# Optimization experiments

Measured on AMD Instinct MI355X. Metric: run time of the kernel, lower is better.

Reference implementation:

```python
import jax, jax.numpy as jnp
import numpy as np

B, N, DIM, HID, MAXN = 2048, 65536, 256, 512, 64
MID_KEY = (MAXN + HID) // 2   # 288
MID_VAL = (DIM + HID) // 2    # 384
MID_DEC = (HID + DIM) // 2    # 384
MID_SZ  = (HID + 1) // 2      # 256

def _ln(x, g, b):
    m = x.mean(-1, keepdims=True)
    v = ((x - m) ** 2).mean(-1, keepdims=True)
    return (x - m) * jax.lax.rsqrt(v + 1e-5) * g + b

def _mish(x):
    return x * jnp.tanh(jax.nn.softplus(x))

def _mlp_ln(x, W1, b1, g, be, W2, b2):
    return _mish(_ln(x @ W1 + b1, g, be)) @ W2 + b2

def _mlp(x, W1, b1, W2, b2):
    return _mish(x @ W1 + b1) @ W2 + b2

def setup_inputs():
    key = jax.random.key(0)
    ks = iter(jax.random.split(key, 40))
    def rn(shape, s=0.05):
        return jax.random.normal(next(ks), shape, jnp.float32) * s
    x = jax.random.normal(next(ks), (N, DIM), jnp.float32)
    batch = jnp.sort(jax.random.randint(next(ks), (N,), 0, B)).astype(jnp.int32)
    z32 = lambda *s: jnp.zeros(s, jnp.float32)
    o32 = lambda *s: jnp.ones(s, jnp.float32)
    return dict(
        x=x, batch=batch, n_batches=B,
        e_rank_W=rn((DIM, 1)), e_rank_b=z32(1),
        e_card_W=rn((1, HID)), e_card_b=z32(HID),
        e_key_W1=rn((MAXN, MID_KEY)), e_key_b1=z32(MID_KEY), e_key_g=o32(MID_KEY), e_key_be=z32(MID_KEY),
        e_key_W2=rn((MID_KEY, HID)), e_key_b2=z32(HID),
        e_val_W1=rn((DIM, MID_VAL)), e_val_b1=z32(MID_VAL), e_val_g=o32(MID_VAL), e_val_be=z32(MID_VAL),
        e_val_W2=rn((MID_VAL, HID)), e_val_b2=z32(HID),
        d_key_W1=rn((MAXN, MID_KEY)), d_key_b1=z32(MID_KEY), d_key_g=o32(MID_KEY), d_key_be=z32(MID_KEY),
        d_key_W2=rn((MID_KEY, HID)), d_key_b2=z32(HID),
        d_dec_W1=rn((HID, MID_DEC)), d_dec_b1=z32(MID_DEC),
        d_dec_W2=rn((MID_DEC, DIM)), d_dec_b2=z32(DIM),
        d_size_W1=rn((HID, MID_SZ)), d_size_b1=z32(MID_SZ), d_size_g=o32(MID_SZ), d_size_be=z32(MID_SZ),
        d_size_W2=rn((MID_SZ, 1)), d_size_b2=z32(1),
    )

def reference(x, batch, n_batches, e_rank_W, e_rank_b, e_card_W, e_card_b,
              e_key_W1, e_key_b1, e_key_g, e_key_be, e_key_W2, e_key_b2,
              e_val_W1, e_val_b1, e_val_g, e_val_be, e_val_W2, e_val_b2,
              d_key_W1, d_key_b1, d_key_g, d_key_be, d_key_W2, d_key_b2,
              d_dec_W1, d_dec_b1, d_dec_W2, d_dec_b2,
              d_size_W1, d_size_b1, d_size_g, d_size_be, d_size_W2, d_size_b2):
    max_n = e_key_W1.shape[0]
    n_pts = x.shape[0]
    # ---- Encoder ----
    n = jax.ops.segment_sum(jnp.ones(n_pts, jnp.float32), batch, num_segments=n_batches).astype(jnp.int32)
    mag = jnp.abs(x @ e_rank_W + e_rank_b)[:, 0]                 # [N]
    sort_key = batch.astype(jnp.float32) * jnp.max(mag) + mag    # sort within each set by |rank|
    idx = jnp.argsort(sort_key)
    xs = x[idx]
    starts = jnp.cumsum(n) - n                                   # per-set offsets (batch is sorted)
    pos_idx = jnp.arange(n_pts) - starts[batch]                  # rank within each set
    pos = jax.nn.one_hot(pos_idx, max_n, dtype=x.dtype)
    y = _mlp_ln(xs, e_val_W1, e_val_b1, e_val_g, e_val_be, e_val_W2, e_val_b2) \
      * _mlp_ln(pos, e_key_W1, e_key_b1, e_key_g, e_key_be, e_key_W2, e_key_b2)
    z = jax.ops.segment_sum(y, batch, num_segments=n_batches) \
      + n.astype(jnp.float32)[:, None] @ e_card_W + e_card_b     # [B, HID]
    # ---- Decoder ----
    n_logits = _mlp_ln(z, d_size_W1, d_size_b1, d_size_g, d_size_be, d_size_W2, d_size_b2)  # [B, 1]
    n_dec = jnp.clip(jnp.round(n_logits[:, 0]), 0, max_n).astype(jnp.int32)
    keys = _mlp_ln(jnp.eye(max_n, dtype=x.dtype),                # onehot positions 0..max_n-1
                   d_key_W1, d_key_b1, d_key_g, d_key_be, d_key_W2, d_key_b2)  # [max_n, HID]
    zp = z[:, None, :] * keys[None, :, :]                        # [B, max_n, HID] (repeat_interleave -> dense+mask)
    xf = _mlp(zp, d_dec_W1, d_dec_b1, d_dec_W2, d_dec_b2)        # [B, max_n, DIM]
    mask = jnp.arange(max_n)[None, :] < n_dec[:, None]           # valid rows per set
    x_out = (xf * mask[..., None].astype(xf.dtype)).reshape(-1, xf.shape[-1])
    batch_out = jnp.repeat(jnp.arange(n_batches, dtype=jnp.int32), max_n)
    return x_out, batch_out, mask.reshape(-1)
```

## Files before the change

### kernel.cpp

```cpp
#include <hip/hip_runtime.h>

#define NPTS   65536
#define NB     2048
#define DIMX   256
#define HIDN   512
#define MAXNN  64
#define MIDK   288
#define MIDV   384
#define MIDD   384
#define MIDS   256

typedef unsigned short ushort_t;
typedef __attribute__((ext_vector_type(8))) short short8;
typedef __attribute__((ext_vector_type(4))) float f32x4;

__device__ __forceinline__ float mishf(float x) {
    float e = __expf(fminf(x, 30.f));
    float n = e * (e + 2.f);
    return x * n * __builtin_amdgcn_rcpf(n + 2.f);
}
__device__ __forceinline__ ushort_t f2bf(float f) {
    unsigned u = __float_as_uint(f);
    u += 0x7fffu + ((u >> 16) & 1u);
    return (ushort_t)(u >> 16);
}
__device__ __forceinline__ float bf2f(ushort_t h) {
    return __uint_as_float(((unsigned)h) << 16);
}
__device__ __forceinline__ void dma16(const void* g, void* lds) {
    __builtin_amdgcn_global_load_lds(
        (const __attribute__((address_space(1))) unsigned int*)g,
        (__attribute__((address_space(3))) unsigned int*)lds, 16, 0, 0);
}

__global__ __launch_bounds__(256)
void k_starts(const int* __restrict__ batch, int* __restrict__ starts,
              unsigned int* __restrict__ maxmag)
{
    int b = blockIdx.x * blockDim.x + threadIdx.x;
    if (b == 0) *maxmag = 0u;
    if (b <= NB) {
        int lo = 0, hi = NPTS;
        while (lo < hi) { int mid = (lo + hi) >> 1; if (batch[mid] < b) lo = mid + 1; else hi = mid; }
        starts[b] = lo;
    }
}

__global__ __launch_bounds__(256)
void k_mag(const float* __restrict__ x, const float* __restrict__ rW,
           const float* __restrict__ rb, float* __restrict__ mag,
           unsigned int* __restrict__ maxmag, ushort_t* __restrict__ xb)
{
    const int lane = threadIdx.x & 63;
    const int wave = threadIdx.x >> 6;
    const int gw = blockIdx.x * 4 + wave;
    float4 wv = *(const float4*)(rW + lane * 4);
    float bias = rb[0];
    float lmax = 0.f;
    for (int pt = gw; pt < NPTS; pt += 16384) {
        float4 xv = *(const float4*)(x + (size_t)pt * DIMX + lane * 4);
        ushort4 u;
        u.x = f2bf(xv.x); u.y = f2bf(xv.y); u.z = f2bf(xv.z); u.w = f2bf(xv.w);
        *(ushort4*)(xb + (size_t)pt * DIMX + lane * 4) = u;
        double d = (double)xv.x * wv.x + (double)xv.y * wv.y
                 + (double)xv.z * wv.z + (double)xv.w * wv.w;
        #pragma unroll
        for (int o = 32; o > 0; o >>= 1) d += __shfl_xor(d, o);
        float s = fabsf((float)(d + (double)bias));
        if (lane == 0) mag[pt] = s;
        lmax = fmaxf(lmax, s);
    }
    __shared__ float wm[4];
    if (lane == 0) wm[wave] = lmax;
    __syncthreads();
    if (threadIdx.x == 0) {
        float m = fmaxf(fmaxf(wm[0], wm[1]), fmaxf(wm[2], wm[3]));
        atomicMax(maxmag, __float_as_uint(m));
    }
}

__global__ __launch_bounds__(256)
void k_rank(const int* __restrict__ batch, const int* __restrict__ starts,
            const float* __restrict__ mag, const unsigned int* __restrict__ maxmag,
            int* __restrict__ kidx)
{
    int i = blockIdx.x * 256 + threadIdx.x;
    if (i >= NPTS) return;
    int b = batch[i];
    int s = starts[b], e = starts[b + 1];
    float M = __uint_as_float(*maxmag);
    float kb = __fmul_rn((float)b, M);
    float ki = __fadd_rn(kb, mag[i]);
    int r = 0;
    for (int j = s; j < e; ++j) {
        float kj = __fadd_rn(kb, mag[j]);
        r += (kj < ki) || (kj == ki && j < i);
    }
    kidx[i] = (r < MAXNN) ? r : MAXNN;
}

__global__ __launch_bounds__(512)
void k_table2(const float* __restrict__ eW1, const float* __restrict__ eb1,
              const float* __restrict__ eg, const float* __restrict__ ebe,
              const float* __restrict__ eW2, const float* __restrict__ eb2,
              const float* __restrict__ dW1, const float* __restrict__ db1,
              const float* __restrict__ dg, const float* __restrict__ dbe,
              const float* __restrict__ dW2, const float* __restrict__ db2,
              float* __restrict__ enc_tbl, float* __restrict__ dec_tbl)
{
    const int row = blockIdx.x;
    const int t = threadIdx.x;
    const float *W1, *b1, *g, *be, *W2, *b2; float* out; int wrow;
    if (row < 65) {
        W1 = eW1; b1 = eb1; g = eg; be = ebe; W2 = eW2; b2 = eb2;
        out = enc_tbl + row * HIDN; wrow = (row < 64) ? row : -1;
    } else {
        int r = row - 65;
        W1 = dW1; b1 = db1; g = dg; be = dbe; W2 = dW2; b2 = db2;
        out = dec_tbl + r * HIDN; wrow = r;
    }
    __shared__ float h[MIDK];
    __shared__ float red[512];
    float v = 0.f;
    if (t < MIDK) v = b1[t] + (wrow >= 0 ? W1[wrow * MIDK + t] : 0.f);
    red[t] = (t < MIDK) ? v : 0.f;
    __syncthreads();
    for (int o = 256; o > 0; o >>= 1) { if (t < o) red[t] += red[t + o]; __syncthreads(); }
    float m = red[0] / (float)MIDK;
    __syncthreads();
    float d = v - m;
    red[t] = (t < MIDK) ? d * d : 0.f;
    __syncthreads();
    for (int o = 256; o > 0; o >>= 1) { if (t < o) red[t] += red[t + o]; __syncthreads(); }
    float rs = rsqrtf(red[0] / (float)MIDK + 1e-5f);
    __syncthreads();
    if (t < MIDK) h[t] = mishf(d * rs * g[t] + be[t]);
    __syncthreads();
    float acc = b2[t];
    #pragma unroll 8
    for (int k = 0; k < MIDK; ++k) acc = fmaf(h[k], W2[k * HIDN + t], acc);
    out[t] = acc;
}

__global__ __launch_bounds__(256)
void k_card(const int* __restrict__ starts, const float* __restrict__ cardW,
            const float* __restrict__ cardb, float* __restrict__ z)
{
    int idx = blockIdx.x * 256 + threadIdx.x;
    int b = idx >> 9, c = idx & 511;
    float n = (float)(starts[b + 1] - starts[b]);
    z[idx] = fmaf(n, cardW[c], cardb[c]);
}

__global__ __launch_bounds__(256)
void k_size(const float* __restrict__ z, const float* __restrict__ W1,
            const float* __restrict__ b1, const float* __restrict__ g,
            const float* __restrict__ be, const float* __restrict__ W2,
            const float* __restrict__ b2, int* __restrict__ ndec)
{
    const int b0 = blockIdx.x * 4, t = threadIdx.x;
    __shared__ float zr[4][HIDN];
    __shared__ float red[4][256];
    #pragma unroll
    for (int gI = 0; gI < 4; ++gI) {
        zr[gI][t] = z[(b0 + gI) * HIDN + t];
        zr[gI][t + 256] = z[(b0 + gI) * HIDN + 256 + t];
    }
    __syncthreads();
    float acc[4];
    float bb1 = b1[t];
    #pragma unroll
    for (int gI = 0; gI < 4; ++gI) acc[gI] = bb1;
    #pragma unroll 8
    for (int k = 0; k < HIDN; ++k) {
        float wv = W1[k * MIDS + t];
        #pragma unroll
        for (int gI = 0; gI < 4; ++gI) acc[gI] = fmaf(zr[gI][k], wv, acc[gI]);
    }
    #pragma unroll
    for (int gI = 0; gI < 4; ++gI) red[gI][t] = acc[gI];
    __syncthreads();
    for (int o = 128; o > 0; o >>= 1) {
        if (t < o) {
            #pragma unroll
            for (int gI = 0; gI < 4; ++gI) red[gI][t] += red[gI][t + o];
        }
        __syncthreads();
    }
    float mm[4];
    #pragma unroll
    for (int gI = 0; gI < 4; ++gI) mm[gI] = red[gI][0] * (1.f / 256.f);
    __syncthreads();
    #pragma unroll
    for (int gI = 0; gI < 4; ++gI) { float d = acc[gI] - mm[gI]; red[gI][t] = d * d; }
    __syncthreads();
    for (int o = 128; o > 0; o >>= 1) {
        if (t < o) {
            #pragma unroll
            for (int gI = 0; gI < 4; ++gI) red[gI][t] += red[gI][t + o];
        }
        __syncthreads();
    }
    float rs[4];
    #pragma unroll
    for (int gI = 0; gI < 4; ++gI) rs[gI] = rsqrtf(red[gI][0] * (1.f / 256.f) + 1e-5f);
    __syncthreads();
    float w2 = W2[t], gg = g[t], bbe = be[t];
    #pragma unroll
    for (int gI = 0; gI < 4; ++gI) {
        float h = mishf((acc[gI] - mm[gI]) * rs[gI] * gg + bbe);
        red[gI][t] = h * w2;
    }
    __syncthreads();
    for (int o = 128; o > 0; o >>= 1) {
        if (t < o) {
            #pragma unroll
            for (int gI = 0; gI < 4; ++gI) red[gI][t] += red[gI][t + o];
        }
        __syncthreads();
    }
    if (t < 4) {
        float logit = red[t][0] + b2[0];
        float n = rintf(logit);
        n = fminf(fmaxf(n, 0.f), 64.f);
        ndec[b0 + t] = (int)n;
    }
}

__global__ __launch_bounds__(256)
void k_compact_pad(const int* __restrict__ ndec, int* __restrict__ rowmap,
                   int* __restrict__ cntpad)
{
    __shared__ int lcnt;
    const int t = threadIdx.x;
    if (t == 0) lcnt = 0;
    __syncthreads();
    for (int b = t; b < NB; b += 256) {
        int n = ndec[b];
        if (n > 0) {
            int base = atomicAdd(&lcnt, n);
            for (int p = 0; p < n; ++p) rowmap[base + p] = b * 64 + p;
        }
    }
    __syncthreads();
    int c = lcnt;
    int pad = (c + 127) & ~127;
    for (int i = c + t; i < pad; i += 256) rowmap[i] = -1;
    if (t == 0) *cntpad = pad;
}

__global__ __launch_bounds__(256)
void k_tail(const int* __restrict__ ndec, float* __restrict__ outb,
            float* __restrict__ outm)
{
    int r = blockIdx.x * 256 + threadIdx.x;
    if (r < NB * MAXNN) {
        outb[r] = (float)(r >> 6);
        outm[r] = ((r & 63) < ndec[r >> 6]) ? 1.f : 0.f;
    }
}

__global__ __launch_bounds__(256)
void k_wt_all(const float* __restrict__ W0, ushort_t* __restrict__ T0,
              const float* __restrict__ W1s, ushort_t* __restrict__ T1,
              const float* __restrict__ W2s, ushort_t* __restrict__ T2,
              const float* __restrict__ W3s, ushort_t* __restrict__ T3)
{
    int idx = blockIdx.x * 256 + threadIdx.x;
    const float* W; ushort_t* T; int N, K, off;
    if (idx < 98304)       { W = W0;  T = T0; K = 256; N = 384; off = idx; }
    else if (idx < 294912) { W = W1s; T = T1; K = 384; N = 512; off = idx - 98304; }
    else if (idx < 491520) { W = W2s; T = T2; K = 512; N = 384; off = idx - 294912; }
    else                   { W = W3s; T = T3; K = 384; N = 256; off = idx - 491520; }
    int k = off / N, n = off - k * N;
    T[(size_t)n * K + k] = f2bf(W[off]);
}

__global__ __launch_bounds__(512, 2)
void k_enc(const ushort_t* __restrict__ A, const ushort_t* __restrict__ B1t,
           const float* __restrict__ b1, const float* __restrict__ g,
           const float* __restrict__ be, const ushort_t* __restrict__ B2t,
           const float* __restrict__ b2, const float* __restrict__ tbl,
           const int* __restrict__ kidx, const int* __restrict__ batch,
           float* __restrict__ zout)
{
    const int m0 = blockIdx.x * 128;
    __shared__ __align__(16) char SMEM[132096];
    ushort_t* slab = (ushort_t*)SMEM;
    ushort_t* As   = slab;
    ushort_t* Bs   = slab + 8192;
    ushort_t* Bs2  = (ushort_t*)(SMEM + 98304);
    float*    yred = (float*)(SMEM + 98304);
    float*    ssum = (float*)(SMEM + 98304);
    float*    ssq  = ssum + 512;
    int*      barr = (int*)(SMEM + 131072);
    int*      karr = barr + 128;

    const int t = threadIdx.x;
    const int l = t & 63;
    const int w = t >> 6;
    const int l4 = (l >> 4) << 2;
    const int drow = l >> 3;
    const int dblk = (l & 7) ^ drow;

    const int wmA = (w >> 2) * 64;
    const int wqA = (w & 3) * 96;
    f32x4 acc[4][6];
    #pragma unroll
    for (int a = 0; a < 4; ++a)
        #pragma unroll
        for (int b = 0; b < 6; ++b) acc[a][b] = (f32x4)0.f;

    for (int k0 = 0; k0 < DIMX; k0 += 64) {
        #pragma unroll
        for (int ii = 0; ii < 2; ++ii) {
            int i = w * 2 + ii;
            dma16(A + (size_t)(m0 + i * 8 + drow) * DIMX + k0 + dblk * 8, &As[i * 512]);
        }
        #pragma unroll
        for (int ii = 0; ii < 6; ++ii) {
            int i = w * 6 + ii;
            dma16(B1t + (size_t)(i * 8 + drow) * DIMX + k0 + dblk * 8, &Bs[i * 512]);
        }
        __syncthreads();
        #pragma unroll
        for (int ks = 0; ks < 2; ++ks) {
            int kq = ks * 4 + (l >> 4);
            short8 af[4], bfr[6];
            #pragma unroll
            for (int fm = 0; fm < 4; ++fm) {
                int row = wmA + fm * 16 + (l & 15);
                af[fm] = *(const short8*)&As[row * 64 + ((kq ^ (row & 7)) << 3)];
            }
            #pragma unroll
            for (int fn = 0; fn < 6; ++fn) {
                int row = wqA + fn * 16 + (l & 15);
                bfr[fn] = *(const short8*)&Bs[row * 64 + ((kq ^ (row & 7)) << 3)];
            }
            #pragma unroll
            for (int fm = 0; fm < 4; ++fm)
                #pragma unroll
                for (int fn = 0; fn < 6; ++fn)
                    acc[fm][fn] = __builtin_amdgcn_mfma_f32_16x16x32_bf16(
                        af[fm], bfr[fn], acc[fm][fn], 0, 0, 0);
        }
        __syncthreads();
    }

    float bb[6], gg[6], bee[6];
    #pragma unroll
    for (int fn = 0; fn < 6; ++fn) {
        int col = wqA + fn * 16 + (l & 15);
        bb[fn] = b1[col]; gg[fn] = g[col]; bee[fn] = be[col];
    }
    #pragma unroll
    for (int fm = 0; fm < 4; ++fm)
        #pragma unroll
        for (int fn = 0; fn < 6; ++fn)
            #pragma unroll
            for (int j = 0; j < 4; ++j) acc[fm][fn][j] += bb[fn];

    #pragma unroll
    for (int fm = 0; fm < 4; ++fm) {
        #pragma unroll
        for (int j = 0; j < 4; ++j) {
            float s = 0.f, q = 0.f;
            #pragma unroll
            for (int fn = 0; fn < 6; ++fn) {
                float v = acc[fm][fn][j];
                s += v; q += v * v;
            }
            #pragma unroll
            for (int o = 1; o < 16; o <<= 1) {
                s += __shfl_xor(s, o);
                q += __shfl_xor(q, o);
            }
            if ((l & 15) == 0) {
                int r = wmA + fm * 16 + l4 + j;
                ssum[r * 4 + (w & 3)] = s;
                ssq[r * 4 + (w & 3)] = q;
            }
        }
    }
    if (t < 128) { barr[t] = batch[m0 + t]; karr[t] = kidx[m0 + t]; }
    __syncthreads();

    #pragma unroll
    for (int fm = 0; fm < 4; ++fm) {
        #pragma unroll
        for (int j = 0; j < 4; ++j) {
            int r = wmA + fm * 16 + l4 + j;
            float s = ssum[r * 4 + 0] + ssum[r * 4 + 1] + ssum[r * 4 + 2] + ssum[r * 4 + 3];
            float q = ssq[r * 4 + 0] + ssq[r * 4 + 1] + ssq[r * 4 + 2] + ssq[r * 4 + 3];
            float m = s * (1.f / 384.f);
            float var = q * (1.f / 384.f) - m * m;
            float rs = rsqrtf(var + 1e-5f);
            #pragma unroll
            for (int fn = 0; fn < 6; ++fn) {
                float v = (acc[fm][fn][j] - m) * rs * gg[fn] + bee[fn];
                int c = wqA + fn * 16 + (l & 15);
                int panel = c >> 6, cc = c & 63;
                int kb = (cc >> 3) ^ (r & 7);
                slab[panel * 8192 + r * 64 + kb * 8 + (cc & 7)] = f2bf(mishf(v));
            }
        }
    }
    __syncthreads();

    const int wmB = (w >> 1) * 32;
    const int wnB = (w & 1) * 64;
    for (int nt = 0; nt < 4; ++nt) {
        const int n0t = nt * 128;
        f32x4 acc2[2][4];
        #pragma unroll
        for (int a = 0; a < 2; ++a)
            #pragma unroll
            for (int b = 0; b < 4; ++b) acc2[a][b] = (f32x4)0.f;

        for (int k0 = 0; k0 < MIDV; k0 += 64) {
            const int panel = k0 >> 6;
            #pragma unroll
            for (int ii = 0; ii < 2; ++ii) {
                int i = w * 2 + ii;
                dma16(B2t + (size_t)(n0t + i * 8 + drow) * MIDV + k0 + dblk * 8,
                      &Bs2[i * 512]);
            }
            __syncthreads();
            #pragma unroll
            for (int ks = 0; ks < 2; ++ks) {
                int kq = ks * 4 + (l >> 4);
                short8 af[2], bfr[4];
                #pragma unroll
                for (int fm = 0; fm < 2; ++fm) {
                    int row = wmB + fm * 16 + (l & 15);
                    af[fm] = *(const short8*)&slab[panel * 8192 + row * 64
                                                   + ((kq ^ (row & 7)) << 3)];
                }
                #pragma unroll
                for (int fn = 0; fn < 4; ++fn) {
                    int row = wnB + fn * 16 + (l & 15);
                    bfr[fn] = *(const short8*)&Bs2[row * 64 + ((kq ^ (row & 7)) << 3)];
                }
                #pragma unroll
                for (int fm = 0; fm < 2; ++fm)
                    #pragma unroll
                    for (int fn = 0; fn < 4; ++fn)
                        acc2[fm][fn] = __builtin_amdgcn_mfma_f32_16x16x32_bf16(
                            af[fm], bfr[fn], acc2[fm][fn], 0, 0, 0);
            }
            __syncthreads();
        }

        #pragma unroll
        for (int ph = 0; ph < 2; ++ph) {
            if ((w >> 2) == ph) {
                int rowbase = ((w >> 1) & 1) * 32;
                #pragma unroll
                for (int fn = 0; fn < 4; ++fn) {
                    int cl = wnB + fn * 16 + (l & 15);
                    float bbv = b2[n0t + cl];
                    #pragma unroll
                    for (int fm = 0; fm < 2; ++fm) {
                        #pragma unroll
                        for (int j = 0; j < 4; ++j) {
                            int rl = rowbase + fm * 16 + l4 + j;
                            int rg = ph * 64 + rl;
                            float v = (acc2[fm][fn][j] + bbv)
                                    * tbl[karr[rg] * HIDN + n0t + cl];
                            yred[cl * 64 + (rl ^ (cl & 31))] = v;
                        }
                    }
                }
            }
            __syncthreads();
            {
                int c = t & 127, q4 = t >> 7;
                int gc = n0t + c;
                float run = 0.f; int curb = -1;
                #pragma unroll 1
                for (int rr = 0; rr < 16; ++rr) {
                    int rl = q4 * 16 + rr;
                    int b = barr[ph * 64 + rl];
                    float v = yred[c * 64 + (rl ^ (c & 31))];
                    if (b != curb) {
                        if (curb >= 0) atomicAdd(&zout[curb * HIDN + gc], run);
                        curb = b; run = v;
                    } else run += v;
                }
                atomicAdd(&zout[curb * HIDN + gc], run);
            }
            __syncthreads();
        }
    }
}

template<int MODE>
__device__ __forceinline__
void mm_body(const ushort_t* __restrict__ A, const ushort_t* __restrict__ Bt,
             const float* __restrict__ bias, void* __restrict__ Cptr, int K,
             const float* __restrict__ tbl, const float* __restrict__ zin,
             const int* __restrict__ rowmap, const int* __restrict__ cntpad)
{
    const int flat = blockIdx.y * gridDim.x + blockIdx.x;
    const int nx = gridDim.x;
    const int xcd = flat & 7;
    const int lin = flat >> 3;
    const int n0 = (lin % nx) * 128;
    const int m0 = ((lin / nx) + ((gridDim.y >> 3) * xcd)) * 128;
    if (m0 >= *cntpad) return;
    __shared__ __align__(16) ushort_t sAB[2 * 128 * 64];
    ushort_t* As = sAB;
    ushort_t* Bs = sAB + 128 * 64;
    const int t = threadIdx.x;
    const int l = t & 63;
    const int w = t >> 6;
    const int wm = (w >> 1) * 64;
    const int wn = (w & 1) * 64;
    const int l4 = (l >> 4) << 2;
    const int drow = l >> 3;
    const int dblk = (l & 7) ^ drow;

    int g4[4], p4[4];
    if (MODE == 2) {
        #pragma unroll
        for (int ii = 0; ii < 4; ++ii) {
            int i = w * 4 + ii;
            int gr = rowmap[m0 + i * 8 + drow];
            if (gr < 0) gr = 0;
            g4[ii] = gr >> 6; p4[ii] = gr & 63;
        }
    }

    f32x4 acc[4][4];
    #pragma unroll
    for (int a = 0; a < 4; ++a)
        #pragma unroll
        for (int b = 0; b < 4; ++b) acc[a][b] = (f32x4)0.f;

    for (int k0 = 0; k0 < K; k0 += 64) {
        if (MODE == 2) {
            #pragma unroll
            for (int ii = 0; ii < 4; ++ii) {
                int i = w * 4 + ii;
                int row = i * 8 + drow;
                const float* zp = zin + g4[ii] * HIDN + k0 + dblk * 8;
                const float* kp = tbl + p4[ii] * HIDN + k0 + dblk * 8;
                float4 z0 = *(const float4*)zp;
                float4 z1 = *(const float4*)(zp + 4);
                float4 q0 = *(const float4*)kp;
                float4 q1 = *(const float4*)(kp + 4);
                ushort4 u0, u1;
                u0.x = f2bf(z0.x * q0.x); u0.y = f2bf(z0.y * q0.y);
                u0.z = f2bf(z0.z * q0.z); u0.w = f2bf(z0.w * q0.w);
                u1.x = f2bf(z1.x * q1.x); u1.y = f2bf(z1.y * q1.y);
                u1.z = f2bf(z1.z * q1.z); u1.w = f2bf(z1.w * q1.w);
                ushort_t* dst = &As[row * 64 + (l & 7) * 8];
                *(ushort4*)dst = u0;
                *(ushort4*)(dst + 4) = u1;
            }
        } else {
            #pragma unroll
            for (int ii = 0; ii < 4; ++ii) {
                int i = w * 4 + ii;
                const ushort_t* gp = A + (size_t)(m0 + i * 8 + drow) * K + k0 + dblk * 8;
                dma16(gp, &As[i * 512]);
            }
        }
        #pragma unroll
        for (int ii = 0; ii < 4; ++ii) {
            int i = w * 4 + ii;
            const ushort_t* gp = Bt + (size_t)(n0 + i * 8 + drow) * K + k0 + dblk * 8;
            dma16(gp, &Bs[i * 512]);
        }
        __syncthreads();
        #pragma unroll
        for (int ks = 0; ks < 2; ++ks) {
            short8 af[4], bfr[4];
            int kq = ks * 4 + (l >> 4);
            #pragma unroll
            for (int fm = 0; fm < 4; ++fm) {
                int row = wm + fm * 16 + (l & 15);
                af[fm] = *(const short8*)&As[row * 64 + ((kq ^ (row & 7)) << 3)];
            }
            #pragma unroll
            for (int fn = 0; fn < 4; ++fn) {
                int row = wn + fn * 16 + (l & 15);
                bfr[fn] = *(const short8*)&Bs[row * 64 + ((kq ^ (row & 7)) << 3)];
            }
            #pragma unroll
            for (int fm = 0; fm < 4; ++fm)
                #pragma unroll
                for (int fn = 0; fn < 4; ++fn)
                    acc[fm][fn] = __builtin_amdgcn_mfma_f32_16x16x32_bf16(
                        af[fm], bfr[fn], acc[fm][fn], 0, 0, 0);
        }
        __syncthreads();
    }

    if (MODE == 2) {
        ushort_t* C = (ushort_t*)Cptr;
        #pragma unroll
        for (int fm = 0; fm < 4; ++fm) {
            int gr0 = m0 + wm + fm * 16 + l4;
            #pragma unroll
            for (int fn = 0; fn < 4; ++fn) {
                int gc = n0 + wn + fn * 16 + (l & 15);
                float bbv = bias[gc];
                #pragma unroll
                for (int j = 0; j < 4; ++j)
                    C[(size_t)(gr0 + j) * MIDD + gc] = f2bf(mishf(acc[fm][fn][j] + bbv));
            }
        }
    } else {
        float* C = (float*)Cptr;
        #pragma unroll
        for (int fm = 0; fm < 4; ++fm) {
            int gr0 = m0 + wm + fm * 16 + l4;
            int om[4];
            #pragma unroll
            for (int j = 0; j < 4; ++j) om[j] = rowmap[gr0 + j];
            #pragma unroll
            for (int fn = 0; fn < 4; ++fn) {
                int gc = n0 + wn + fn * 16 + (l & 15);
                float bbv = bias[gc];
                #pragma unroll
                for (int j = 0; j < 4; ++j)
                    if (om[j] >= 0) C[(size_t)om[j] * DIMX + gc] = acc[fm][fn][j] + bbv;
            }
        }
    }
}

__global__ __launch_bounds__(256, 2)
void k_mm_d1(const ushort_t* Bt, const float* bias, void* C, int K,
             const float* tbl, const float* zin, const int* rowmap, const int* cntpad)
{ mm_body<2>(nullptr, Bt, bias, C, K, tbl, zin, rowmap, cntpad); }

__global__ __launch_bounds__(256, 2)
void k_mm_d2(const ushort_t* A, const ushort_t* Bt, const float* bias, void* C, int K,
             const int* rowmap, const int* cntpad)
{ mm_body<3>(A, Bt, bias, C, K, nullptr, nullptr, rowmap, cntpad); }

extern "C" void kernel_launch(void* const* d_in, const int* in_sizes, int n_in,
                              void* d_out, int out_size, void* d_ws, size_t ws_size,
                              hipStream_t stream)
{
    const float* x        = (const float*)d_in[0];
    const int*   batch    = (const int*)  d_in[1];
    const float* e_rank_W = (const float*)d_in[3];
    const float* e_rank_b = (const float*)d_in[4];
    const float* e_card_W = (const float*)d_in[5];
    const float* e_card_b = (const float*)d_in[6];
    const float* e_key_W1 = (const float*)d_in[7];
    const float* e_key_b1 = (const float*)d_in[8];
    const float* e_key_g  = (const float*)d_in[9];
    const float* e_key_be = (const float*)d_in[10];
    const float* e_key_W2 = (const float*)d_in[11];
    const float* e_key_b2 = (const float*)d_in[12];
    const float* e_val_W1 = (const float*)d_in[13];
    const float* e_val_b1 = (const float*)d_in[14];
    const float* e_val_g  = (const float*)d_in[15];
    const float* e_val_be = (const float*)d_in[16];
    const float* e_val_W2 = (const float*)d_in[17];
    const float* e_val_b2 = (const float*)d_in[18];
    const float* d_key_W1 = (const float*)d_in[19];
    const float* d_key_b1 = (const float*)d_in[20];
    const float* d_key_g  = (const float*)d_in[21];
    const float* d_key_be = (const float*)d_in[22];
    const float* d_key_W2 = (const float*)d_in[23];
    const float* d_key_b2 = (const float*)d_in[24];
    const float* d_dec_W1 = (const float*)d_in[25];
    const float* d_dec_b1 = (const float*)d_in[26];
    const float* d_dec_W2 = (const float*)d_in[27];
    const float* d_dec_b2 = (const float*)d_in[28];
    const float* d_size_W1= (const float*)d_in[29];
    const float* d_size_b1= (const float*)d_in[30];
    const float* d_size_g = (const float*)d_in[31];
    const float* d_size_be= (const float*)d_in[32];
    const float* d_size_W2= (const float*)d_in[33];
    const float* d_size_b2= (const float*)d_in[34];

    char* ws = (char*)d_ws;
    int*          starts  = (int*)         (ws + 0);
    unsigned int* maxmag  = (unsigned int*)(ws + 8448);
    int*          kidx    = (int*)         (ws + 8704);
    float*        mag     = (float*)       (ws + 270848);
    float*        enc_tbl = (float*)       (ws + 532992);
    float*        dec_tbl = (float*)       (ws + 666112);
    float*        z       = (float*)       (ws + 797184);
    int*          ndec    = (int*)         (ws + 4991488);
    int*          cntpad  = (int*)         (ws + 4999684);
    int*          rowmap  = (int*)         (ws + 5000192);
    ushort_t*     evW1t   = (ushort_t*)    (ws + 5524480);
    ushort_t*     evW2t   = (ushort_t*)    (ws + 5721088);
    ushort_t*     ddW1t   = (ushort_t*)    (ws + 6114304);
    ushort_t*     ddW2t   = (ushort_t*)    (ws + 6507520);
    ushort_t*     xb      = (ushort_t*)    (ws + 6704384);
    ushort_t*     Hd      = (ushort_t*)    (ws + 6704384 + 33554432);

    float* out_x = (float*)d_out;
    float* out_b = out_x + (size_t)NB * MAXNN * DIMX;
    float* out_m = out_b + NB * MAXNN;

    hipMemsetAsync(out_x, 0, (size_t)NB * MAXNN * DIMX * sizeof(float), stream);
    k_starts<<<dim3(9), dim3(256), 0, stream>>>(batch, starts, maxmag);
    k_mag<<<dim3(4096), dim3(256), 0, stream>>>(x, e_rank_W, e_rank_b, mag, maxmag, xb);
    k_rank<<<dim3(256), dim3(256), 0, stream>>>(batch, starts, mag, maxmag, kidx);
    k_table2<<<dim3(129), dim3(512), 0, stream>>>(
        e_key_W1, e_key_b1, e_key_g, e_key_be, e_key_W2, e_key_b2,
        d_key_W1, d_key_b1, d_key_g, d_key_be, d_key_W2, d_key_b2,
        enc_tbl, dec_tbl);
    k_card<<<dim3(4096), dim3(256), 0, stream>>>(starts, e_card_W, e_card_b, z);
    k_wt_all<<<dim3(2304), dim3(256), 0, stream>>>(e_val_W1, evW1t, e_val_W2, evW2t,
                                                   d_dec_W1, ddW1t, d_dec_W2, ddW2t);

    k_enc<<<dim3(512), dim3(512), 0, stream>>>(xb, evW1t, e_val_b1, e_val_g, e_val_be,
                                               evW2t, e_val_b2, enc_tbl, kidx, batch, z);

    k_size<<<dim3(NB / 4), dim3(256), 0, stream>>>(z, d_size_W1, d_size_b1, d_size_g,
                                                   d_size_be, d_size_W2, d_size_b2, ndec);
    k_compact_pad<<<dim3(1), dim3(256), 0, stream>>>(ndec, rowmap, cntpad);
    k_mm_d1<<<dim3(3, 1024), dim3(256), 0, stream>>>(ddW1t, d_dec_b1, Hd, HIDN,
                                                     dec_tbl, z, rowmap, cntpad);
    k_mm_d2<<<dim3(2, 1024), dim3(256), 0, stream>>>(Hd, ddW2t, d_dec_b2, out_x, MIDD,
                                                     rowmap, cntpad);
    k_tail<<<dim3(512), dim3(256), 0, stream>>>(ndec, out_b, out_m);
}
```

Measured before the change: 523.3 us.

## Merge setup kernels, inline segment bounds, widen encoder K step, batch segment-sum reads

```diff
diff --git a/kernel.cpp b/kernel.cpp
--- a/kernel.cpp
+++ b/kernel.cpp
@@ -32,18 +32,9 @@
         (const __attribute__((address_space(1))) unsigned int*)g,
         (__attribute__((address_space(3))) unsigned int*)lds, 16, 0, 0);
 }
-
-__global__ __launch_bounds__(256)
-void k_starts(const int* __restrict__ batch, int* __restrict__ starts,
-              unsigned int* __restrict__ maxmag)
-{
-    int b = blockIdx.x * blockDim.x + threadIdx.x;
-    if (b == 0) *maxmag = 0u;
-    if (b <= NB) {
-        int lo = 0, hi = NPTS;
-        while (lo < hi) { int mid = (lo + hi) >> 1; if (batch[mid] < b) lo = mid + 1; else hi = mid; }
-        starts[b] = lo;
-    }
+__device__ __forceinline__ int lbound(const int* __restrict__ a, int lo, int hi, int v) {
+    while (lo < hi) { int m = (lo + hi) >> 1; if (a[m] < v) lo = m + 1; else hi = m; }
+    return lo;
 }
 
 __global__ __launch_bounds__(256)
@@ -80,14 +71,14 @@
 }
 
 __global__ __launch_bounds__(256)
-void k_rank(const int* __restrict__ batch, const int* __restrict__ starts,
-            const float* __restrict__ mag, const unsigned int* __restrict__ maxmag,
-            int* __restrict__ kidx)
+void k_rank(const int* __restrict__ batch, const float* __restrict__ mag,
+            const unsigned int* __restrict__ maxmag, int* __restrict__ kidx)
 {
     int i = blockIdx.x * 256 + threadIdx.x;
     if (i >= NPTS) return;
     int b = batch[i];
-    int s = starts[b], e = starts[b + 1];
+    int s = lbound(batch, 0, NPTS, b);
+    int e = lbound(batch, s, NPTS, b + 1);
     float M = __uint_as_float(*maxmag);
     float kb = __fmul_rn((float)b, M);
     float ki = __fadd_rn(kb, mag[i]);
@@ -100,56 +91,69 @@
 }
 
 __global__ __launch_bounds__(512)
-void k_table2(const float* __restrict__ eW1, const float* __restrict__ eb1,
-              const float* __restrict__ eg, const float* __restrict__ ebe,
-              const float* __restrict__ eW2, const float* __restrict__ eb2,
-              const float* __restrict__ dW1, const float* __restrict__ db1,
-              const float* __restrict__ dg, const float* __restrict__ dbe,
-              const float* __restrict__ dW2, const float* __restrict__ db2,
-              float* __restrict__ enc_tbl, float* __restrict__ dec_tbl)
-{
-    const int row = blockIdx.x;
+void k_setup(const float* __restrict__ eW1, const float* __restrict__ eb1,
+             const float* __restrict__ eg, const float* __restrict__ ebe,
+             const float* __restrict__ eW2, const float* __restrict__ eb2,
+             const float* __restrict__ dW1, const float* __restrict__ db1,
+             const float* __restrict__ dg, const float* __restrict__ dbe,
+             const float* __restrict__ dW2, const float* __restrict__ db2,
+             float* __restrict__ enc_tbl, float* __restrict__ dec_tbl,
+             const int* __restrict__ batch, const float* __restrict__ cardW,
+             const float* __restrict__ cardb, float* __restrict__ z,
+             const float* __restrict__ V0, ushort_t* __restrict__ T0,
+             const float* __restrict__ V1, ushort_t* __restrict__ T1,
+             const float* __restrict__ V2, ushort_t* __restrict__ T2,
+             const float* __restrict__ V3, ushort_t* __restrict__ T3)
+{
+    const int blk = blockIdx.x;
     const int t = threadIdx.x;
-    const float *W1, *b1, *g, *be, *W2, *b2; float* out; int wrow;
-    if (row < 65) {
-        W1 = eW1; b1 = eb1; g = eg; be = ebe; W2 = eW2; b2 = eb2;
-        out = enc_tbl + row * HIDN; wrow = (row < 64) ? row : -1;
+    if (blk < 129) {
+        const float *W1, *b1, *g, *be, *W2, *b2; float* out; int wrow;
+        if (blk < 65) {
+            W1 = eW1; b1 = eb1; g = eg; be = ebe; W2 = eW2; b2 = eb2;
+            out = enc_tbl + blk * HIDN; wrow = (blk < 64) ? blk : -1;
+        } else {
+            int r = blk - 65;
+            W1 = dW1; b1 = db1; g = dg; be = dbe; W2 = dW2; b2 = db2;
+            out = dec_tbl + r * HIDN; wrow = r;
+        }
+        __shared__ float h[MIDK];
+        __shared__ float red[512];
+        float v = 0.f;
+        if (t < MIDK) v = b1[t] + (wrow >= 0 ? W1[wrow * MIDK + t] : 0.f);
+        red[t] = (t < MIDK) ? v : 0.f;
+        __syncthreads();
+        for (int o = 256; o > 0; o >>= 1) { if (t < o) red[t] += red[t + o]; __syncthreads(); }
+        float m = red[0] / (float)MIDK;
+        __syncthreads();
+        float d = v - m;
+        red[t] = (t < MIDK) ? d * d : 0.f;
+        __syncthreads();
+        for (int o = 256; o > 0; o >>= 1) { if (t < o) red[t] += red[t + o]; __syncthreads(); }
+        float rs = rsqrtf(red[0] / (float)MIDK + 1e-5f);
+        __syncthreads();
+        if (t < MIDK) h[t] = mishf(d * rs * g[t] + be[t]);
+        __syncthreads();
+        float acc = b2[t];
+        #pragma unroll 8
+        for (int k = 0; k < MIDK; ++k) acc = fmaf(h[k], W2[k * HIDN + t], acc);
+        out[t] = acc;
+    } else if (blk < 129 + NB) {
+        int b = blk - 129;
+        int s = lbound(batch, 0, NPTS, b);
+        int e = lbound(batch, s, NPTS, b + 1);
+        float n = (float)(e - s);
+        z[b * HIDN + t] = fmaf(n, cardW[t], cardb[t]);
     } else {
-        int r = row - 65;
-        W1 = dW1; b1 = db1; g = dg; be = dbe; W2 = dW2; b2 = db2;
-        out = dec_tbl + r * HIDN; wrow = r;
-    }
-    __shared__ float h[MIDK];
-    __shared__ float red[512];
-    float v = 0.f;
-    if (t < MIDK) v = b1[t] + (wrow >= 0 ? W1[wrow * MIDK + t] : 0.f);
-    red[t] = (t < MIDK) ? v : 0.f;
-    __syncthreads();
-    for (int o = 256; o > 0; o >>= 1) { if (t < o) red[t] += red[t + o]; __syncthreads(); }
-    float m = red[0] / (float)MIDK;
-    __syncthreads();
-    float d = v - m;
-    red[t] = (t < MIDK) ? d * d : 0.f;
-    __syncthreads();
-    for (int o = 256; o > 0; o >>= 1) { if (t < o) red[t] += red[t + o]; __syncthreads(); }
-    float rs = rsqrtf(red[0] / (float)MIDK + 1e-5f);
-    __syncthreads();
-    if (t < MIDK) h[t] = mishf(d * rs * g[t] + be[t]);
-    __syncthreads();
-    float acc = b2[t];
-    #pragma unroll 8
-    for (int k = 0; k < MIDK; ++k) acc = fmaf(h[k], W2[k * HIDN + t], acc);
-    out[t] = acc;
-}
-
-__global__ __launch_bounds__(256)
-void k_card(const int* __restrict__ starts, const float* __restrict__ cardW,
-            const float* __restrict__ cardb, float* __restrict__ z)
-{
-    int idx = blockIdx.x * 256 + threadIdx.x;
-    int b = idx >> 9, c = idx & 511;
-    float n = (float)(starts[b + 1] - starts[b]);
-    z[idx] = fmaf(n, cardW[c], cardb[c]);
+        int idx = (blk - (129 + NB)) * 512 + t;
+        const float* W; ushort_t* T; int N, K, off;
+        if (idx < 98304)       { W = V0; T = T0; K = 256; N = 384; off = idx; }
+        else if (idx < 294912) { W = V1; T = T1; K = 384; N = 512; off = idx - 98304; }
+        else if (idx < 491520) { W = V2; T = T2; K = 512; N = 384; off = idx - 294912; }
+        else                   { W = V3; T = T3; K = 384; N = 256; off = idx - 491520; }
+        int k = off / N, n = off - k * N;
+        T[(size_t)n * K + k] = f2bf(W[off]);
+    }
 }
 
 __global__ __launch_bounds__(256)
@@ -258,22 +262,6 @@
         outb[r] = (float)(r >> 6);
         outm[r] = ((r & 63) < ndec[r >> 6]) ? 1.f : 0.f;
     }
-}
-
-__global__ __launch_bounds__(256)
-void k_wt_all(const float* __restrict__ W0, ushort_t* __restrict__ T0,
-              const float* __restrict__ W1s, ushort_t* __restrict__ T1,
-              const float* __restrict__ W2s, ushort_t* __restrict__ T2,
-              const float* __restrict__ W3s, ushort_t* __restrict__ T3)
-{
-    int idx = blockIdx.x * 256 + threadIdx.x;
-    const float* W; ushort_t* T; int N, K, off;
-    if (idx < 98304)       { W = W0;  T = T0; K = 256; N = 384; off = idx; }
-    else if (idx < 294912) { W = W1s; T = T1; K = 384; N = 512; off = idx - 98304; }
-    else if (idx < 491520) { W = W2s; T = T2; K = 512; N = 384; off = idx - 294912; }
-    else                   { W = W3s; T = T3; K = 384; N = 256; off = idx - 491520; }
-    int k = off / N, n = off - k * N;
-    T[(size_t)n * K + k] = f2bf(W[off]);
 }
 
 __global__ __launch_bounds__(512, 2)
@@ -417,29 +405,32 @@
             #pragma unroll
             for (int b = 0; b < 4; ++b) acc2[a][b] = (f32x4)0.f;
 
-        for (int k0 = 0; k0 < MIDV; k0 += 64) {
-            const int panel = k0 >> 6;
-            #pragma unroll
-            for (int ii = 0; ii < 2; ++ii) {
-                int i = w * 2 + ii;
-                dma16(B2t + (size_t)(n0t + i * 8 + drow) * MIDV + k0 + dblk * 8,
-                      &Bs2[i * 512]);
+        for (int k0 = 0; k0 < MIDV; k0 += 128) {
+            #pragma unroll
+            for (int ii = 0; ii < 4; ++ii) {
+                int pp = ii >> 1;
+                int i = w * 2 + (ii & 1);
+                dma16(B2t + (size_t)(n0t + i * 8 + drow) * MIDV + k0 + pp * 64 + dblk * 8,
+                      &Bs2[pp * 8192 + i * 512]);
             }
             __syncthreads();
             #pragma unroll
-            for (int ks = 0; ks < 2; ++ks) {
+            for (int ks = 0; ks < 4; ++ks) {
                 int kq = ks * 4 + (l >> 4);
+                int pp = kq >> 3, kb = kq & 7;
+                int panel = (k0 >> 6) + pp;
                 short8 af[2], bfr[4];
                 #pragma unroll
                 for (int fm = 0; fm < 2; ++fm) {
                     int row = wmB + fm * 16 + (l & 15);
                     af[fm] = *(const short8*)&slab[panel * 8192 + row * 64
-                                                   + ((kq ^ (row & 7)) << 3)];
+                                                   + ((kb ^ (row & 7)) << 3)];
                 }
                 #pragma unroll
                 for (int fn = 0; fn < 4; ++fn) {
                     int row = wnB + fn * 16 + (l & 15);
-                    bfr[fn] = *(const short8*)&Bs2[row * 64 + ((kq ^ (row & 7)) << 3)];
+                    bfr[fn] = *(const short8*)&Bs2[pp * 8192 + row * 64
+                                                   + ((kb ^ (row & 7)) << 3)];
                 }
                 #pragma unroll
                 for (int fm = 0; fm < 2; ++fm)
@@ -473,19 +464,27 @@
                 }
             }
             __syncthreads();
-            {
-                int c = t & 127, q4 = t >> 7;
+            if (t < 256) {
+                int c = t & 127, q = t >> 7;
                 int gc = n0t + c;
+                int base = q * 32;
                 float run = 0.f; int curb = -1;
-                #pragma unroll 1
-                for (int rr = 0; rr < 16; ++rr) {
-                    int rl = q4 * 16 + rr;
-                    int b = barr[ph * 64 + rl];
-                    float v = yred[c * 64 + (rl ^ (c & 31))];
-                    if (b != curb) {
-                        if (curb >= 0) atomicAdd(&zout[curb * HIDN + gc], run);
-                        curb = b; run = v;
-                    } else run += v;
+                #pragma unroll
+                for (int ch = 0; ch < 2; ++ch) {
+                    float v16[16]; int b16[16];
+                    #pragma unroll
+                    for (int rr = 0; rr < 16; ++rr) {
+                        int rl = base + ch * 16 + rr;
+                        v16[rr] = yred[c * 64 + (rl ^ (c & 31))];
+                        b16[rr] = barr[ph * 64 + rl];
+                    }
+                    #pragma unroll
+                    for (int rr = 0; rr < 16; ++rr) {
+                        if (b16[rr] != curb) {
+                            if (curb >= 0) atomicAdd(&zout[curb * HIDN + gc], run);
+                            curb = b16[rr]; run = v16[rr];
+                        } else run += v16[rr];
+                    }
                 }
                 atomicAdd(&zout[curb * HIDN + gc], run);
             }
@@ -681,7 +680,6 @@
     const float* d_size_b2= (const float*)d_in[34];
 
     char* ws = (char*)d_ws;
-    int*          starts  = (int*)         (ws + 0);
     unsigned int* maxmag  = (unsigned int*)(ws + 8448);
     int*          kidx    = (int*)         (ws + 8704);
     float*        mag     = (float*)       (ws + 270848);
@@ -703,16 +701,14 @@
     float* out_m = out_b + NB * MAXNN;
 
     hipMemsetAsync(out_x, 0, (size_t)NB * MAXNN * DIMX * sizeof(float), stream);
-    k_starts<<<dim3(9), dim3(256), 0, stream>>>(batch, starts, maxmag);
+    hipMemsetAsync(maxmag, 0, 4, stream);
     k_mag<<<dim3(4096), dim3(256), 0, stream>>>(x, e_rank_W, e_rank_b, mag, maxmag, xb);
-    k_rank<<<dim3(256), dim3(256), 0, stream>>>(batch, starts, mag, maxmag, kidx);
-    k_table2<<<dim3(129), dim3(512), 0, stream>>>(
+    k_rank<<<dim3(256), dim3(256), 0, stream>>>(batch, mag, maxmag, kidx);
+    k_setup<<<dim3(129 + NB + 1152), dim3(512), 0, stream>>>(
         e_key_W1, e_key_b1, e_key_g, e_key_be, e_key_W2, e_key_b2,
         d_key_W1, d_key_b1, d_key_g, d_key_be, d_key_W2, d_key_b2,
-        enc_tbl, dec_tbl);
-    k_card<<<dim3(4096), dim3(256), 0, stream>>>(starts, e_card_W, e_card_b, z);
-    k_wt_all<<<dim3(2304), dim3(256), 0, stream>>>(e_val_W1, evW1t, e_val_W2, evW2t,
-                                                   d_dec_W1, ddW1t, d_dec_W2, ddW2t);
+        enc_tbl, dec_tbl, batch, e_card_W, e_card_b, z,
+        e_val_W1, evW1t, e_val_W2, evW2t, d_dec_W1, ddW1t, d_dec_W2, ddW2t);
 
     k_enc<<<dim3(512), dim3(512), 0, stream>>>(xb, evW1t, e_val_b1, e_val_g, e_val_be,
                                                evW2t, e_val_b2, enc_tbl, kidx, batch, z);
```

Measured after the change: 505.5 us. 1.04x faster.
